# Kernel tuning notes

Hardware: AMD Instinct MI355X
Metric: run time of the kernel (lower is better)

The kernel has to match this reference:

```python
import jax, jax.numpy as jnp
import numpy as np


def setup_inputs() -> dict:
    key = jax.random.key(0)
    k1, k2, k3, k4 = jax.random.split(key, 4)
    B, S, IN, OUT = 4, 2048, 4096, 4096
    x = jax.random.normal(k1, (B, S, IN), dtype=jnp.float32)
    # 4-bit signed range [-8, 7], stored widened (torch uses int8)
    weight_quantized = jax.random.randint(k2, (OUT, IN), -8, 8, dtype=jnp.int32)
    # per-output-row scale, positive and small (abs-max / 7 style)
    weight_scale = jax.random.uniform(k3, (OUT,), dtype=jnp.float32) * 0.01 + 1e-4
    bias = jax.random.normal(k4, (OUT,), dtype=jnp.float32) * 0.01
    return {"x": x, "weight_quantized": weight_quantized,
            "weight_scale": weight_scale, "bias": bias}


def reference(x, weight_quantized, weight_scale, bias):
    # dequantize: [OUT, IN] int -> fp32 scaled per output row
    w = weight_quantized.astype(jnp.float32) * weight_scale[:, None]
    # F.linear: x @ w.T + bias  -> [B, S, OUT]
    out = jnp.einsum('bsi,oi->bso', x, w) + bias
    return out
```

## Files before the change

kernel.cpp:

```cpp
#include <hip/hip_runtime.h>
#include <hip/hip_bf16.h>

typedef __bf16 bf16x4 __attribute__((ext_vector_type(4)));
typedef __bf16 bf16x8 __attribute__((ext_vector_type(8)));
typedef float  floatx4 __attribute__((ext_vector_type(4)));

#define AS1 __attribute__((address_space(1)))
#define AS3 __attribute__((address_space(3)))

__global__ __launch_bounds__(256)
void cvt_both4(const float* __restrict__ xin, const int* __restrict__ win,
               __bf16* __restrict__ xout, __bf16* __restrict__ wout,
               int nx4, int nw4)
{
    int i = blockIdx.x * 256 + threadIdx.x;
    if (i < nx4) {
        float4 a = reinterpret_cast<const float4*>(xin)[i];
        bf16x4 h;
        h[0] = (__bf16)a.x; h[1] = (__bf16)a.y;
        h[2] = (__bf16)a.z; h[3] = (__bf16)a.w;
        reinterpret_cast<bf16x4*>(xout)[i] = h;
    } else {
        int j = i - nx4;
        if (j < nw4) {
            int4 a = reinterpret_cast<const int4*>(win)[j];
            bf16x4 h;
            h[0] = (__bf16)(float)a.x; h[1] = (__bf16)(float)a.y;
            h[2] = (__bf16)(float)a.z; h[3] = (__bf16)(float)a.w;
            reinterpret_cast<bf16x4*>(wout)[j] = h;
        }
    }
}

#define BM2 256
#define BN2 256
#define BK2 64

template<int P>
__device__ __forceinline__ void phase_mfma(const __bf16* cA, const bf16x8 (&bfr)[4][2],
                                           floatx4 (&acc)[8][4],
                                           int wm, int lm, int kq, int sw)
{
    bf16x8 af[2][2];
#pragma unroll
    for (int ii = 0; ii < 2; ++ii)
#pragma unroll
        for (int h = 0; h < 2; ++h)
            af[ii][h] = *reinterpret_cast<const bf16x8*>(
                &cA[(wm + (2 * P + ii) * 16 + lm) * BK2 + ((kq + h * 4) ^ sw) * 8]);
    __builtin_amdgcn_s_setprio(1);
#pragma unroll
    for (int h = 0; h < 2; ++h)
#pragma unroll
        for (int ii = 0; ii < 2; ++ii)
#pragma unroll
            for (int j = 0; j < 4; ++j)
                acc[2 * P + ii][j] = __builtin_amdgcn_mfma_f32_16x16x32_bf16(
                                         af[ii][h], bfr[j][h], acc[2 * P + ii][j], 0, 0, 0);
    __builtin_amdgcn_s_setprio(0);
    asm volatile("s_barrier" ::: "memory");
}

__global__ __launch_bounds__(512)
void gemm_bf16_bt_8ph(const __bf16* __restrict__ A, const __bf16* __restrict__ B,
                      const float* __restrict__ scale, const float* __restrict__ bias,
                      float* __restrict__ Out, int M, int N, int K)
{
    __shared__ __bf16 sA[2][BM2 * BK2];
    __shared__ __bf16 sB[2][BN2 * BK2];

    const int tid  = threadIdx.x;
    const int wave = tid >> 6;
    const int lane = tid & 63;
    const int row0 = blockIdx.y * BM2;
    const int col0 = blockIdx.x * BN2;

    const int sRow = lane >> 3;
    const int gBlk = (lane & 7) ^ sRow;
    const size_t aBase = (size_t)(row0 + wave * 8 + sRow) * K + gBlk * 8;
    const size_t bBase = (size_t)(col0 + wave * 8 + sRow) * K + gBlk * 8;
    const int ldsWOff = wave * 8 * BK2;

#define STAGE_A(buf, q, kt_) \
    __builtin_amdgcn_global_load_lds( \
        (const AS1 void*)(A + aBase + (size_t)(q) * 64 * K + (size_t)(kt_) * BK2), \
        (AS3 void*)&sA[(buf)][(q) * 64 * BK2 + ldsWOff], 16, 0, 0)
#define STAGE_B(buf, q, kt_) \
    __builtin_amdgcn_global_load_lds( \
        (const AS1 void*)(B + bBase + (size_t)(q) * 64 * K + (size_t)(kt_) * BK2), \
        (AS3 void*)&sB[(buf)][(q) * 64 * BK2 + ldsWOff], 16, 0, 0)

    const int wm = (wave >> 2) * 128;
    const int wn = (wave & 3) * 64;
    const int lm = lane & 15;
    const int kq = lane >> 4;
    const int sw = lm & 7;

    floatx4 acc[8][4];
#pragma unroll
    for (int i = 0; i < 8; ++i)
#pragma unroll
        for (int j = 0; j < 4; ++j)
            acc[i][j] = (floatx4)0.0f;

    const int nt = K / BK2;

    STAGE_A(0, 0, 0); STAGE_A(0, 1, 0); STAGE_A(0, 2, 0); STAGE_A(0, 3, 0);
    STAGE_B(0, 0, 0); STAGE_B(0, 1, 0); STAGE_B(0, 2, 0); STAGE_B(0, 3, 0);
    STAGE_A(1, 0, 1); STAGE_A(1, 2, 1);

    for (int kt = 0; kt < nt; ++kt) {
        const int c  = kt & 1;
        const int n1 = (kt + 1 < nt) ? kt + 1 : 0;
        const int n2 = (kt + 2 < nt) ? kt + 2 : 0;
        const __bf16* cA = sA[c];
        const __bf16* cB = sB[c];

        STAGE_A(c ^ 1, 1, n1); STAGE_A(c ^ 1, 3, n1);
        asm volatile("s_waitcnt vmcnt(4)" ::: "memory");
        asm volatile("s_barrier" ::: "memory");

        bf16x8 bfr[4][2];
#pragma unroll
        for (int j = 0; j < 4; ++j)
#pragma unroll
            for (int h = 0; h < 2; ++h)
                bfr[j][h] = *reinterpret_cast<const bf16x8*>(
                    &cB[(wn + j * 16 + lm) * BK2 + ((kq + h * 4) ^ sw) * 8]);
        phase_mfma<0>(cA, bfr, acc, wm, lm, kq, sw);

        STAGE_B(c ^ 1, 0, n1); STAGE_B(c ^ 1, 1, n1);
        STAGE_B(c ^ 1, 2, n1); STAGE_B(c ^ 1, 3, n1);
        phase_mfma<1>(cA, bfr, acc, wm, lm, kq, sw);

        STAGE_A(c, 0, n2); STAGE_A(c, 2, n2);
        phase_mfma<2>(cA, bfr, acc, wm, lm, kq, sw);

        phase_mfma<3>(cA, bfr, acc, wm, lm, kq, sw);
    }

#pragma unroll
    for (int j = 0; j < 4; ++j) {
        int n = col0 + wn + j * 16 + lm;
        float sc = scale[n];
        float bi = bias[n];
#pragma unroll
        for (int i = 0; i < 8; ++i) {
#pragma unroll
            for (int r = 0; r < 4; ++r) {
                int m = row0 + wm + i * 16 + kq * 4 + r;
                Out[(size_t)m * N + n] = sc * acc[i][j][r] + bi;
            }
        }
    }
#undef STAGE_A
#undef STAGE_B
}

#define BM 128
#define BN 128
#define BK 64

__global__ __launch_bounds__(256)
void gemm_bf16_bt(const __bf16* __restrict__ A, const __bf16* __restrict__ B,
                  const float* __restrict__ scale, const float* __restrict__ bias,
                  float* __restrict__ Out, int M, int N, int K)
{
    __shared__ __bf16 sA[BM * BK];
    __shared__ __bf16 sB[BN * BK];

    const int tid  = threadIdx.x;
    const int row0 = blockIdx.y * BM;
    const int col0 = blockIdx.x * BN;
    const int wave = tid >> 6;
    const int lane = tid & 63;

    const int sRow = lane >> 3;
    const int gBlk = (lane & 7) ^ sRow;
    size_t aOff[4], bOff[4];
    const __bf16* ldsA[4];
    const __bf16* ldsB[4];
#pragma unroll
    for (int q = 0; q < 4; ++q) {
        int r = wave * 32 + q * 8 + sRow;
        aOff[q] = (size_t)(row0 + r) * K + gBlk * 8;
        bOff[q] = (size_t)(col0 + r) * K + gBlk * 8;
        ldsA[q] = &sA[(wave * 32 + q * 8) * BK];
        ldsB[q] = &sB[(wave * 32 + q * 8) * BK];
    }

    const int wm = (wave >> 1) * 64;
    const int wn = (wave & 1) * 64;
    const int lm = lane & 15;
    const int kq = lane >> 4;
    const int sw = lm & 7;

    floatx4 acc[4][4];
#pragma unroll
    for (int i = 0; i < 4; ++i)
#pragma unroll
        for (int j = 0; j < 4; ++j)
            acc[i][j] = (floatx4)0.0f;

    for (int k0 = 0; k0 < K; k0 += BK) {
#pragma unroll
        for (int q = 0; q < 4; ++q) {
            __builtin_amdgcn_global_load_lds((const AS1 void*)(A + aOff[q] + k0),
                                             (AS3 void*)ldsA[q], 16, 0, 0);
            __builtin_amdgcn_global_load_lds((const AS1 void*)(B + bOff[q] + k0),
                                             (AS3 void*)ldsB[q], 16, 0, 0);
        }
        __syncthreads();

#pragma unroll
        for (int h = 0; h < 2; ++h) {
            const int blkA = (kq + h * 4);
            bf16x8 af[4], bfr[4];
#pragma unroll
            for (int i = 0; i < 4; ++i) {
                int row = wm + i * 16 + lm;
                af[i] = *reinterpret_cast<const bf16x8*>(
                            &sA[row * BK + (blkA ^ sw) * 8]);
            }
#pragma unroll
            for (int j = 0; j < 4; ++j) {
                int row = wn + j * 16 + lm;
                bfr[j] = *reinterpret_cast<const bf16x8*>(
                            &sB[row * BK + (blkA ^ sw) * 8]);
            }
#pragma unroll
            for (int i = 0; i < 4; ++i)
#pragma unroll
                for (int j = 0; j < 4; ++j)
                    acc[i][j] = __builtin_amdgcn_mfma_f32_16x16x32_bf16(
                                    af[i], bfr[j], acc[i][j], 0, 0, 0);
        }
        __syncthreads();
    }

#pragma unroll
    for (int j = 0; j < 4; ++j) {
        int n = col0 + wn + j * 16 + lm;
        float sc = scale[n];
        float bi = bias[n];
#pragma unroll
        for (int i = 0; i < 4; ++i) {
#pragma unroll
            for (int r = 0; r < 4; ++r) {
                int m = row0 + wm + i * 16 + kq * 4 + r;
                Out[(size_t)m * N + n] = sc * acc[i][j][r] + bi;
            }
        }
    }
}

__global__ __launch_bounds__(256)
void fp4linear_gemm(const float* __restrict__ X, const int* __restrict__ W,
                    const float* __restrict__ scale, const float* __restrict__ bias,
                    float* __restrict__ Out, int M, int N, int K)
{
    __shared__ __bf16 sA[BM * 32];
    __shared__ __bf16 sB[BN * 32];

    const int tid  = threadIdx.x;
    const int row0 = blockIdx.y * BM;
    const int col0 = blockIdx.x * BN;
    const int wave = tid >> 6;
    const int lane = tid & 63;
    const int wm = (wave >> 1) * 64;
    const int wn = (wave & 1) * 64;
    const int lm = lane & 15;
    const int kq = lane >> 4;

    floatx4 acc[4][4];
#pragma unroll
    for (int i = 0; i < 4; ++i)
#pragma unroll
        for (int j = 0; j < 4; ++j)
            acc[i][j] = (floatx4)0.0f;

    for (int k0 = 0; k0 < K; k0 += 32) {
        float4 fa[4];
        int4   ib[4];
#pragma unroll
        for (int l = 0; l < 4; ++l) {
            int idx = tid + l * 256;
            int r = idx >> 3, c4 = idx & 7;
            fa[l] = *reinterpret_cast<const float4*>(
                        &X[(size_t)(row0 + r) * K + k0 + c4 * 4]);
        }
#pragma unroll
        for (int l = 0; l < 4; ++l) {
            int idx = tid + l * 256;
            int r = idx >> 3, c4 = idx & 7;
            ib[l] = *reinterpret_cast<const int4*>(
                        &W[(size_t)(col0 + r) * K + k0 + c4 * 4]);
        }
        __syncthreads();
#pragma unroll
        for (int l = 0; l < 4; ++l) {
            int idx = tid + l * 256;
            int r = idx >> 3, c4 = idx & 7;
            bf16x4 h;
            h[0] = (__bf16)fa[l].x; h[1] = (__bf16)fa[l].y;
            h[2] = (__bf16)fa[l].z; h[3] = (__bf16)fa[l].w;
            *reinterpret_cast<bf16x4*>(&sA[r * 32 + c4 * 4]) = h;
        }
#pragma unroll
        for (int l = 0; l < 4; ++l) {
            int idx = tid + l * 256;
            int r = idx >> 3, c4 = idx & 7;
            bf16x4 h;
            h[0] = (__bf16)(float)ib[l].x; h[1] = (__bf16)(float)ib[l].y;
            h[2] = (__bf16)(float)ib[l].z; h[3] = (__bf16)(float)ib[l].w;
            *reinterpret_cast<bf16x4*>(&sB[r * 32 + c4 * 4]) = h;
        }
        __syncthreads();

        bf16x8 af[4], bfr[4];
#pragma unroll
        for (int i = 0; i < 4; ++i)
            af[i] = *reinterpret_cast<const bf16x8*>(
                        &sA[(wm + i * 16 + lm) * 32 + kq * 8]);
#pragma unroll
        for (int j = 0; j < 4; ++j)
            bfr[j] = *reinterpret_cast<const bf16x8*>(
                        &sB[(wn + j * 16 + lm) * 32 + kq * 8]);
#pragma unroll
        for (int i = 0; i < 4; ++i)
#pragma unroll
            for (int j = 0; j < 4; ++j)
                acc[i][j] = __builtin_amdgcn_mfma_f32_16x16x32_bf16(
                                af[i], bfr[j], acc[i][j], 0, 0, 0);
    }

#pragma unroll
    for (int j = 0; j < 4; ++j) {
        int n = col0 + wn + j * 16 + lm;
        float sc = scale[n];
        float bi = bias[n];
#pragma unroll
        for (int i = 0; i < 4; ++i) {
#pragma unroll
            for (int r = 0; r < 4; ++r) {
                int m = row0 + wm + i * 16 + kq * 4 + r;
                Out[(size_t)m * N + n] = sc * acc[i][j][r] + bi;
            }
        }
    }
}

extern "C" void kernel_launch(void* const* d_in, const int* in_sizes, int n_in,
                              void* d_out, int out_size, void* d_ws, size_t ws_size,
                              hipStream_t stream) {
    const float* x     = (const float*)d_in[0];
    const int*   wq    = (const int*)d_in[1];
    const float* scale = (const float*)d_in[2];
    const float* bias  = (const float*)d_in[3];
    float* out = (float*)d_out;

    const int N = in_sizes[2];
    const int K = in_sizes[1] / N;
    const int M = in_sizes[0] / K;

    const size_t xElems = (size_t)M * K;
    const size_t wElems = (size_t)N * K;
    const size_t need   = (xElems + wElems) * sizeof(__bf16);

    const bool cvt_ok = (ws_size >= need) && (xElems % 4 == 0) && (wElems % 4 == 0);

    if (cvt_ok && (M % BM2 == 0) && (N % BN2 == 0) && (K % BK2 == 0)) {
        __bf16* xb = (__bf16*)d_ws;
        __bf16* wb = xb + xElems;
        int nx4 = (int)(xElems / 4);
        int nw4 = (int)(wElems / 4);
        int total = nx4 + nw4;
        hipLaunchKernelGGL(cvt_both4, dim3((total + 255) / 256), dim3(256), 0, stream,
                           x, wq, xb, wb, nx4, nw4);
        hipLaunchKernelGGL(gemm_bf16_bt_8ph, dim3(N / BN2, M / BM2), dim3(512), 0, stream,
                           xb, wb, scale, bias, out, M, N, K);
    } else if (cvt_ok && (M % BM == 0) && (N % BN == 0) && (K % BK == 0)) {
        __bf16* xb = (__bf16*)d_ws;
        __bf16* wb = xb + xElems;
        int nx4 = (int)(xElems / 4);
        int nw4 = (int)(wElems / 4);
        int total = nx4 + nw4;
        hipLaunchKernelGGL(cvt_both4, dim3((total + 255) / 256), dim3(256), 0, stream,
                           x, wq, xb, wb, nx4, nw4);
        hipLaunchKernelGGL(gemm_bf16_bt, dim3(N / BN, M / BM), dim3(256), 0, stream,
                           xb, wb, scale, bias, out, M, N, K);
    } else {
        hipLaunchKernelGGL(fp4linear_gemm, dim3(N / BN, M / BM), dim3(256), 0, stream,
                           x, wq, scale, bias, out, M, N, K);
    }
}
```

Baseline: 570.1 us.

## Unroll GEMM K-loop by two and prefetch next B fragments during last phase

The bf16 GEMM main loop is unrolled two K-tiles at a time with fixed LDS buffers. The B-fragment registers for the next tile are loaded from LDS during the final MFMA phase of the current tile, so that LDS read latency is hidden behind compute instead of sitting after the barrier. The conversion kernel now handles 8 elements per thread in a grid-stride loop with a capped block count. This adds register pressure from two B fragment sets and a stricter requirement that the number of K tiles be even.

```diff
diff --git a/kernel.cpp b/kernel.cpp
--- a/kernel.cpp
+++ b/kernel.cpp
@@ -9,25 +9,30 @@
 #define AS3 __attribute__((address_space(3)))
 
 __global__ __launch_bounds__(256)
-void cvt_both4(const float* __restrict__ xin, const int* __restrict__ win,
+void cvt_both8(const float* __restrict__ xin, const int* __restrict__ win,
                __bf16* __restrict__ xout, __bf16* __restrict__ wout,
-               int nx4, int nw4)
-{
-    int i = blockIdx.x * 256 + threadIdx.x;
-    if (i < nx4) {
-        float4 a = reinterpret_cast<const float4*>(xin)[i];
-        bf16x4 h;
-        h[0] = (__bf16)a.x; h[1] = (__bf16)a.y;
-        h[2] = (__bf16)a.z; h[3] = (__bf16)a.w;
-        reinterpret_cast<bf16x4*>(xout)[i] = h;
-    } else {
-        int j = i - nx4;
-        if (j < nw4) {
-            int4 a = reinterpret_cast<const int4*>(win)[j];
-            bf16x4 h;
+               int nx8, int nw8)
+{
+    const int stride = gridDim.x * 256;
+    const int total  = nx8 + nw8;
+    for (int i = blockIdx.x * 256 + threadIdx.x; i < total; i += stride) {
+        if (i < nx8) {
+            const float4* p = reinterpret_cast<const float4*>(xin) + (size_t)i * 2;
+            float4 a = p[0], b = p[1];
+            bf16x8 h;
+            h[0] = (__bf16)a.x; h[1] = (__bf16)a.y; h[2] = (__bf16)a.z; h[3] = (__bf16)a.w;
+            h[4] = (__bf16)b.x; h[5] = (__bf16)b.y; h[6] = (__bf16)b.z; h[7] = (__bf16)b.w;
+            reinterpret_cast<bf16x8*>(xout)[i] = h;
+        } else {
+            int j = i - nx8;
+            const int4* p = reinterpret_cast<const int4*>(win) + (size_t)j * 2;
+            int4 a = p[0], b = p[1];
+            bf16x8 h;
             h[0] = (__bf16)(float)a.x; h[1] = (__bf16)(float)a.y;
             h[2] = (__bf16)(float)a.z; h[3] = (__bf16)(float)a.w;
-            reinterpret_cast<bf16x4*>(wout)[j] = h;
+            h[4] = (__bf16)(float)b.x; h[5] = (__bf16)(float)b.y;
+            h[6] = (__bf16)(float)b.z; h[7] = (__bf16)(float)b.w;
+            reinterpret_cast<bf16x8*>(wout)[j] = h;
         }
     }
 }
@@ -37,9 +42,9 @@
 #define BK2 64
 
 template<int P>
-__device__ __forceinline__ void phase_mfma(const __bf16* cA, const bf16x8 (&bfr)[4][2],
-                                           floatx4 (&acc)[8][4],
-                                           int wm, int lm, int kq, int sw)
+__device__ __forceinline__ void phaseAB(const __bf16* cA, const bf16x8 (&bfr)[4][2],
+                                        floatx4 (&acc)[8][4],
+                                        int wm, int lm, int kq, int sw)
 {
     bf16x8 af[2][2];
 #pragma unroll
@@ -58,13 +63,44 @@
                 acc[2 * P + ii][j] = __builtin_amdgcn_mfma_f32_16x16x32_bf16(
                                          af[ii][h], bfr[j][h], acc[2 * P + ii][j], 0, 0, 0);
     __builtin_amdgcn_s_setprio(0);
-    asm volatile("s_barrier" ::: "memory");
-}
+}
+
+__device__ __forceinline__ void phase3(const __bf16* cA, const __bf16* cBn,
+                                       const bf16x8 (&bfr)[4][2], bf16x8 (&bfrN)[4][2],
+                                       floatx4 (&acc)[8][4],
+                                       int wm, int wn, int lm, int kq, int sw)
+{
+    bf16x8 af[2][2];
+#pragma unroll
+    for (int ii = 0; ii < 2; ++ii)
+#pragma unroll
+        for (int h = 0; h < 2; ++h)
+            af[ii][h] = *reinterpret_cast<const bf16x8*>(
+                &cA[(wm + (6 + ii) * 16 + lm) * BK2 + ((kq + h * 4) ^ sw) * 8]);
+#pragma unroll
+    for (int j = 0; j < 4; ++j)
+#pragma unroll
+        for (int h = 0; h < 2; ++h)
+            bfrN[j][h] = *reinterpret_cast<const bf16x8*>(
+                &cBn[(wn + j * 16 + lm) * BK2 + ((kq + h * 4) ^ sw) * 8]);
+    __builtin_amdgcn_s_setprio(1);
+#pragma unroll
+    for (int h = 0; h < 2; ++h)
+#pragma unroll
+        for (int ii = 0; ii < 2; ++ii)
+#pragma unroll
+            for (int j = 0; j < 4; ++j)
+                acc[6 + ii][j] = __builtin_amdgcn_mfma_f32_16x16x32_bf16(
+                                     af[ii][h], bfr[j][h], acc[6 + ii][j], 0, 0, 0);
+    __builtin_amdgcn_s_setprio(0);
+}
+
+#define BARRIER() asm volatile("s_barrier" ::: "memory")
 
 __global__ __launch_bounds__(512)
-void gemm_bf16_bt_8ph(const __bf16* __restrict__ A, const __bf16* __restrict__ B,
-                      const float* __restrict__ scale, const float* __restrict__ bias,
-                      float* __restrict__ Out, int M, int N, int K)
+void gemm_bf16_bt_pipe(const __bf16* __restrict__ A, const __bf16* __restrict__ B,
+                       const float* __restrict__ scale, const float* __restrict__ bias,
+                       float* __restrict__ Out, int M, int N, int K)
 {
     __shared__ __bf16 sA[2][BM2 * BK2];
     __shared__ __bf16 sB[2][BN2 * BK2];
@@ -103,41 +139,54 @@
         for (int j = 0; j < 4; ++j)
             acc[i][j] = (floatx4)0.0f;
 
+    bf16x8 bfrA[4][2], bfrB[4][2];
     const int nt = K / BK2;
 
     STAGE_A(0, 0, 0); STAGE_A(0, 1, 0); STAGE_A(0, 2, 0); STAGE_A(0, 3, 0);
     STAGE_B(0, 0, 0); STAGE_B(0, 1, 0); STAGE_B(0, 2, 0); STAGE_B(0, 3, 0);
     STAGE_A(1, 0, 1); STAGE_A(1, 2, 1);
-
-    for (int kt = 0; kt < nt; ++kt) {
-        const int c  = kt & 1;
-        const int n1 = (kt + 1 < nt) ? kt + 1 : 0;
+    asm volatile("s_waitcnt vmcnt(2)" ::: "memory");
+    BARRIER();
+#pragma unroll
+    for (int j = 0; j < 4; ++j)
+#pragma unroll
+        for (int h = 0; h < 2; ++h)
+            bfrA[j][h] = *reinterpret_cast<const bf16x8*>(
+                &sB[0][(wn + j * 16 + lm) * BK2 + ((kq + h * 4) ^ sw) * 8]);
+
+    for (int it = 0; it < nt / 2; ++it) {
+        const int kt = 2 * it;
+        const int n1 = kt + 1;
         const int n2 = (kt + 2 < nt) ? kt + 2 : 0;
-        const __bf16* cA = sA[c];
-        const __bf16* cB = sB[c];
-
-        STAGE_A(c ^ 1, 1, n1); STAGE_A(c ^ 1, 3, n1);
-        asm volatile("s_waitcnt vmcnt(4)" ::: "memory");
-        asm volatile("s_barrier" ::: "memory");
-
-        bf16x8 bfr[4][2];
-#pragma unroll
-        for (int j = 0; j < 4; ++j)
-#pragma unroll
-            for (int h = 0; h < 2; ++h)
-                bfr[j][h] = *reinterpret_cast<const bf16x8*>(
-                    &cB[(wn + j * 16 + lm) * BK2 + ((kq + h * 4) ^ sw) * 8]);
-        phase_mfma<0>(cA, bfr, acc, wm, lm, kq, sw);
-
-        STAGE_B(c ^ 1, 0, n1); STAGE_B(c ^ 1, 1, n1);
-        STAGE_B(c ^ 1, 2, n1); STAGE_B(c ^ 1, 3, n1);
-        phase_mfma<1>(cA, bfr, acc, wm, lm, kq, sw);
-
-        STAGE_A(c, 0, n2); STAGE_A(c, 2, n2);
-        phase_mfma<2>(cA, bfr, acc, wm, lm, kq, sw);
-
-        phase_mfma<3>(cA, bfr, acc, wm, lm, kq, sw);
-    }
+        const int n3 = (kt + 3 < nt) ? kt + 3 : 0;
+
+        STAGE_A(1, 1, n1); STAGE_A(1, 3, n1);
+        phaseAB<0>(sA[0], bfrA, acc, wm, lm, kq, sw);
+        BARRIER();
+        STAGE_B(1, 0, n1); STAGE_B(1, 1, n1); STAGE_B(1, 2, n1); STAGE_B(1, 3, n1);
+        phaseAB<1>(sA[0], bfrA, acc, wm, lm, kq, sw);
+        BARRIER();
+        STAGE_A(0, 0, n2); STAGE_A(0, 2, n2);
+        phaseAB<2>(sA[0], bfrA, acc, wm, lm, kq, sw);
+        asm volatile("s_waitcnt vmcnt(2)" ::: "memory");
+        BARRIER();
+        phase3(sA[0], sB[1], bfrA, bfrB, acc, wm, wn, lm, kq, sw);
+        BARRIER();
+
+        STAGE_A(0, 1, n2); STAGE_A(0, 3, n2);
+        phaseAB<0>(sA[1], bfrB, acc, wm, lm, kq, sw);
+        BARRIER();
+        STAGE_B(0, 0, n2); STAGE_B(0, 1, n2); STAGE_B(0, 2, n2); STAGE_B(0, 3, n2);
+        phaseAB<1>(sA[1], bfrB, acc, wm, lm, kq, sw);
+        BARRIER();
+        STAGE_A(1, 0, n3); STAGE_A(1, 2, n3);
+        phaseAB<2>(sA[1], bfrB, acc, wm, lm, kq, sw);
+        asm volatile("s_waitcnt vmcnt(2)" ::: "memory");
+        BARRIER();
+        phase3(sA[1], sB[0], bfrB, bfrA, acc, wm, wn, lm, kq, sw);
+        BARRIER();
+    }
+    asm volatile("s_waitcnt vmcnt(0)" ::: "memory");
 
 #pragma unroll
     for (int j = 0; j < 4; ++j) {
@@ -367,28 +416,30 @@
     const size_t wElems = (size_t)N * K;
     const size_t need   = (xElems + wElems) * sizeof(__bf16);
 
-    const bool cvt_ok = (ws_size >= need) && (xElems % 4 == 0) && (wElems % 4 == 0);
-
-    if (cvt_ok && (M % BM2 == 0) && (N % BN2 == 0) && (K % BK2 == 0)) {
+    const bool cvt_ok = (ws_size >= need) && (xElems % 8 == 0) && (wElems % 8 == 0);
+    const int  nt     = K / BK2;
+
+    if (cvt_ok) {
         __bf16* xb = (__bf16*)d_ws;
         __bf16* wb = xb + xElems;
-        int nx4 = (int)(xElems / 4);
-        int nw4 = (int)(wElems / 4);
-        int total = nx4 + nw4;
-        hipLaunchKernelGGL(cvt_both4, dim3((total + 255) / 256), dim3(256), 0, stream,
-                           x, wq, xb, wb, nx4, nw4);
-        hipLaunchKernelGGL(gemm_bf16_bt_8ph, dim3(N / BN2, M / BM2), dim3(512), 0, stream,
-                           xb, wb, scale, bias, out, M, N, K);
-    } else if (cvt_ok && (M % BM == 0) && (N % BN == 0) && (K % BK == 0)) {
-        __bf16* xb = (__bf16*)d_ws;
-        __bf16* wb = xb + xElems;
-        int nx4 = (int)(xElems / 4);
-        int nw4 = (int)(wElems / 4);
-        int total = nx4 + nw4;
-        hipLaunchKernelGGL(cvt_both4, dim3((total + 255) / 256), dim3(256), 0, stream,
-                           x, wq, xb, wb, nx4, nw4);
-        hipLaunchKernelGGL(gemm_bf16_bt, dim3(N / BN, M / BM), dim3(256), 0, stream,
-                           xb, wb, scale, bias, out, M, N, K);
+        int nx8 = (int)(xElems / 8);
+        int nw8 = (int)(wElems / 8);
+        int total = nx8 + nw8;
+        int cvtBlocks = (total + 255) / 256;
+        if (cvtBlocks > 2048) cvtBlocks = 2048;
+        hipLaunchKernelGGL(cvt_both8, dim3(cvtBlocks), dim3(256), 0, stream,
+                           x, wq, xb, wb, nx8, nw8);
+        if ((M % BM2 == 0) && (N % BN2 == 0) && (K % BK2 == 0) &&
+            (nt % 2 == 0) && (nt >= 4)) {
+            hipLaunchKernelGGL(gemm_bf16_bt_pipe, dim3(N / BN2, M / BM2), dim3(512),
+                               0, stream, xb, wb, scale, bias, out, M, N, K);
+        } else if ((M % BM == 0) && (N % BN == 0) && (K % BK == 0)) {
+            hipLaunchKernelGGL(gemm_bf16_bt, dim3(N / BN, M / BM), dim3(256),
+                               0, stream, xb, wb, scale, bias, out, M, N, K);
+        } else {
+            hipLaunchKernelGGL(fp4linear_gemm, dim3(N / BN, M / BM), dim3(256),
+                               0, stream, x, wq, scale, bias, out, M, N, K);
+        }
     } else {
         hipLaunchKernelGGL(fp4linear_gemm, dim3(N / BN, M / BM), dim3(256), 0, stream,
                            x, wq, scale, bias, out, M, N, K);
```

After: 545.3 us. -4.3%, faster.
